# Performance work log

Measured on AMD Instinct MI355X. Metric: run time of the kernel, lower is better.

## Reference

```python
import jax, jax.numpy as jnp
import numpy as np

PAD = 0
N_WORDS, INPUT, HIDDEN, LATENT = 32000, 512, 1024, 512
B, T = 64, 512


def setup_inputs() -> dict:
    key = jax.random.key(0)
    ks = jax.random.split(key, 10)
    gin = INPUT + LATENT
    s_ih = 1.0 / np.sqrt(HIDDEN)
    inp = {
        'x': jax.random.randint(ks[0], (B, T), 0, N_WORDS, dtype=jnp.int64) if jax.config.read('jax_enable_x64') else jax.random.randint(ks[0], (B, T), 0, N_WORDS).astype(jnp.int32),
        'z': jax.random.normal(ks[1], (B, LATENT), dtype=jnp.float32),
        'emb_table': jax.random.normal(ks[2], (N_WORDS, INPUT), dtype=jnp.float32) * 0.02,
        'W_ih': jax.random.uniform(ks[3], (3 * HIDDEN, gin), minval=-s_ih, maxval=s_ih, dtype=jnp.float32),
        'b_ih': jax.random.uniform(ks[4], (3 * HIDDEN,), minval=-s_ih, maxval=s_ih, dtype=jnp.float32),
        'W_hh': jax.random.uniform(ks[5], (3 * HIDDEN, HIDDEN), minval=-s_ih, maxval=s_ih, dtype=jnp.float32),
        'b_hh': jax.random.uniform(ks[6], (3 * HIDDEN,), minval=-s_ih, maxval=s_ih, dtype=jnp.float32),
        'W_out': jax.random.uniform(ks[7], (INPUT, HIDDEN + INPUT), minval=-0.02, maxval=0.02, dtype=jnp.float32),
        'b_out': jnp.zeros((INPUT,), dtype=jnp.float32),
    }
    return inp


def _masked_gru(inp, mask, W_ih, b_ih, W_hh, b_hh):
    # inp: [B,T,Din], mask: [B,T] True at PAD positions (hidden frozen there)
    x_proj = jnp.einsum('btd,gd->btg', inp, W_ih) + b_ih  # [B,T,3H]
    xp = jnp.swapaxes(x_proj, 0, 1)                       # [T,B,3H]
    m = jnp.swapaxes(mask, 0, 1)                          # [T,B]
    h0 = jnp.zeros((inp.shape[0], HIDDEN), dtype=inp.dtype)

    def step(h, xm):
        xp_t, m_t = xm
        hp = h @ W_hh.T + b_hh
        xr, xu, xn = jnp.split(xp_t, 3, axis=-1)
        hr, hu, hn = jnp.split(hp, 3, axis=-1)
        r = jax.nn.sigmoid(xr + hr)
        u = jax.nn.sigmoid(xu + hu)
        n = jnp.tanh(xn + r * hn)
        h_new = (1.0 - u) * n + u * h
        h = jnp.where(m_t[:, None], h, h_new)
        return h, h

    _, hs = jax.lax.scan(step, h0, (xp, m))
    return jnp.swapaxes(hs, 0, 1)  # [B,T,H]


def reference(x, z, emb_table, W_ih, b_ih, W_hh, b_hh, W_out, b_out):
    mask = (x == PAD)                                  # [B,T]
    emb = emb_table[x]                                 # [B,T,INPUT]
    zt = jnp.broadcast_to(z[:, None, :], (x.shape[0], x.shape[1], z.shape[-1]))
    inp = jnp.concatenate([emb, zt], axis=-1)          # [B,T,INPUT+LATENT]
    hidden = _masked_gru(inp, mask, W_ih, b_ih, W_hh, b_hh)
    cat = jnp.concatenate([hidden, emb], axis=-1)      # [B,T,H+INPUT]
    logits = jnp.tanh(jnp.einsum('btd,od->bto', cat, W_out) + b_out)
    return logits
```

## Files before the change

### kernel.cpp

```cpp
#include <hip/hip_runtime.h>
#include <cmath>

#define PAD 0
#define INPUT 512
#define HIDDEN 1024
#define LATENT 512
#define BATCH 64
#define TLEN 512
#define G3 3072
#define GIN 1024
#define NXCD 8
#define TC 64

__global__ __launch_bounds__(256) void k_zproj(const float* __restrict__ z,
                                               const float* __restrict__ W_ih,
                                               const float* __restrict__ b_ih,
                                               float* __restrict__ zp) {
    __shared__ float zs[LATENT];
    const int b = blockIdx.y;
    const int g = blockIdx.x * 256 + threadIdx.x;
    for (int i = threadIdx.x; i < LATENT; i += 256) zs[i] = z[b * LATENT + i];
    __syncthreads();
    const float* wrow = W_ih + (size_t)g * GIN + INPUT;
    float acc = b_ih[g];
#pragma unroll 4
    for (int k = 0; k < LATENT; k += 4) {
        const float4 w = *reinterpret_cast<const float4*>(wrow + k);
        acc += zs[k] * w.x + zs[k + 1] * w.y + zs[k + 2] * w.z + zs[k + 3] * w.w;
    }
    zp[b * G3 + g] = acc;
}

__global__ void k_mask(const int* __restrict__ x, int* __restrict__ maskT) {
    const int t = blockIdx.x;
    const int b = threadIdx.x;
    maskT[t * BATCH + b] = (x[b * TLEN + t] == PAD) ? 1 : 0;
}

__global__ __launch_bounds__(256) void k_xproj(const int* __restrict__ x,
                                               const float* __restrict__ emb,
                                               const float* __restrict__ W_ih,
                                               const float* __restrict__ zp,
                                               float* __restrict__ xp,
                                               const int t_base) {
    __shared__ float smem[8448];
    __shared__ int toks[128];
    float (*As)[132] = (float(*)[132])smem;
    float (*Bs)[68]  = (float(*)[68])(smem + 4224);
    float (*Cs)[132] = (float(*)[132])smem;

    const int tid = threadIdx.x;
    const int tx = tid & 15, ty = tid >> 4;
    const int n0 = blockIdx.x * 64;
    const int m0 = blockIdx.y * 128;
    const int t0 = m0 >> 6;
    if (tid < 128) toks[tid] = x[(tid & 63) * TLEN + t_base + t0 + (tid >> 6)];
    __syncthreads();

    float acc[8][4] = {};
    for (int k0 = 0; k0 < INPUT; k0 += 32) {
        for (int idx = tid; idx < 128 * 32; idx += 256) {
            const int i = idx >> 5, kk = idx & 31;
            As[kk][i] = emb[(size_t)toks[i] * INPUT + k0 + kk];
        }
        for (int idx = tid; idx < 64 * 32; idx += 256) {
            const int i = idx >> 5, kk = idx & 31;
            Bs[kk][i] = W_ih[(size_t)(n0 + i) * GIN + k0 + kk];
        }
        __syncthreads();
#pragma unroll
        for (int kk = 0; kk < 32; ++kk) {
            const float4 a0 = *reinterpret_cast<const float4*>(&As[kk][ty * 8]);
            const float4 a1 = *reinterpret_cast<const float4*>(&As[kk][ty * 8 + 4]);
            const float4 bv = *reinterpret_cast<const float4*>(&Bs[kk][tx * 4]);
            const float av[8] = {a0.x, a0.y, a0.z, a0.w, a1.x, a1.y, a1.z, a1.w};
            const float bw[4] = {bv.x, bv.y, bv.z, bv.w};
#pragma unroll
            for (int i = 0; i < 8; ++i)
#pragma unroll
                for (int j = 0; j < 4; ++j) acc[i][j] += av[i] * bw[j];
        }
        __syncthreads();
    }
#pragma unroll
    for (int i = 0; i < 8; ++i) {
        const int b = (ty * 8 + i) & 63;
        const float4 zv = *reinterpret_cast<const float4*>(&zp[(size_t)b * G3 + n0 + tx * 4]);
        Cs[tx * 4 + 0][ty * 8 + i] = acc[i][0] + zv.x;
        Cs[tx * 4 + 1][ty * 8 + i] = acc[i][1] + zv.y;
        Cs[tx * 4 + 2][ty * 8 + i] = acc[i][2] + zv.z;
        Cs[tx * 4 + 3][ty * 8 + i] = acc[i][3] + zv.w;
    }
    __syncthreads();
#pragma unroll
    for (int it = 0; it < 32; ++it) {
        const int idx = it * 256 + tid;
        const int b = idx & 63;
        const int gl = (idx >> 6) & 63;
        const int tt = idx >> 12;
        xp[(size_t)(t0 + tt) * (G3 * BATCH) + (size_t)(n0 + gl) * BATCH + b] =
            Cs[gl][tt * 64 + b];
    }
}

__global__ __launch_bounds__(256) void k_gru_step(
    const float* __restrict__ xp_t,
    const float* __restrict__ hrep_r,
    float* __restrict__ hrep_w,
    float* __restrict__ hs_t,
    const float* __restrict__ Whh,
    const float* __restrict__ bhh,
    const int* __restrict__ maskt,
    const int t) {
    __shared__ float Ws[12 * 1024];
    __shared__ float Ab[2 * 64 * 128];

    const int tid = threadIdx.x;
    const int jl = tid >> 6;
    const int b = tid & 63;
    const int j0 = blockIdx.x * 4;
    const int j = j0 + jl;

    const float xr = xp_t[(size_t)j * BATCH + b];
    const float xu = xp_t[(size_t)(HIDDEN + j) * BATCH + b];
    const float xn = xp_t[(size_t)(2 * HIDDEN + j) * BATCH + b];
    const float* hrd = hrep_r + (size_t)(blockIdx.x & (NXCD - 1)) * (BATCH * HIDDEN);
    const float hold = (t > 0) ? hrd[b * HIDDEN + j] : 0.f;
    const int msk = maskt[b];
    const float br = bhh[j], bu = bhh[HIDDEN + j], bn = bhh[2 * HIDDEN + j];

#pragma unroll
    for (int q = 0; q < 12; ++q) {
        const int f4 = q * 256 + tid;
        const int row = f4 >> 8;
        const int col = (f4 & 255) * 4;
        const int g = (row >> 2) * HIDDEN + j0 + (row & 3);
        *reinterpret_cast<float4*>(&Ws[row * 1024 + col]) =
            *reinterpret_cast<const float4*>(&Whh[(size_t)g * HIDDEN + col]);
    }

    float ar0 = 0.f, ar1 = 0.f, au0 = 0.f, au1 = 0.f, an0 = 0.f, an1 = 0.f;

    if (t > 0) {
        float4 st[8];
        auto ldchunk = [&](int c, float4* r) {
#pragma unroll
            for (int q = 0; q < 8; ++q) {
                const int flat = q * 256 + tid;
                const int bb = flat >> 5;
                const int kc = (flat & 31) * 4;
                const int ks = kc ^ ((bb & 7) << 2);
                r[q] = *reinterpret_cast<const float4*>(
                    &hrd[(size_t)bb * HIDDEN + c * 128 + ks]);
            }
        };
        auto stchunk = [&](int buf, const float4* r) {
            float* A = Ab + buf * (64 * 128);
#pragma unroll
            for (int q = 0; q < 8; ++q) {
                const int flat = q * 256 + tid;
                *reinterpret_cast<float4*>(&A[flat * 4]) = r[q];
            }
        };

        ldchunk(0, st);
        stchunk(0, st);
        __syncthreads();

        const int swz = (b & 7) << 2;
        const float* wrb = Ws + (0 * 4 + jl) * 1024;
        const float* wub = Ws + (4 + jl) * 1024;
        const float* wnb = Ws + (8 + jl) * 1024;

        for (int c = 0; c < 8; ++c) {
            if (c < 7) ldchunk(c + 1, st);
            const float* A = Ab + (c & 1) * (64 * 128) + b * 128;
            const float* wr = wrb + c * 128;
            const float* wu = wub + c * 128;
            const float* wn = wnb + c * 128;
#pragma unroll
            for (int kk = 0; kk < 128; kk += 8) {
                const float4 h0 = *reinterpret_cast<const float4*>(&A[kk ^ swz]);
                const float4 h1 = *reinterpret_cast<const float4*>(&A[(kk + 4) ^ swz]);
                const float4 r0 = *reinterpret_cast<const float4*>(&wr[kk]);
                const float4 r1 = *reinterpret_cast<const float4*>(&wr[kk + 4]);
                const float4 u0 = *reinterpret_cast<const float4*>(&wu[kk]);
                const float4 u1 = *reinterpret_cast<const float4*>(&wu[kk + 4]);
                const float4 n0v = *reinterpret_cast<const float4*>(&wn[kk]);
                const float4 n1v = *reinterpret_cast<const float4*>(&wn[kk + 4]);
                ar0 += h0.x * r0.x + h0.y * r0.y + h0.z * r0.z + h0.w * r0.w;
                ar1 += h1.x * r1.x + h1.y * r1.y + h1.z * r1.z + h1.w * r1.w;
                au0 += h0.x * u0.x + h0.y * u0.y + h0.z * u0.z + h0.w * u0.w;
                au1 += h1.x * u1.x + h1.y * u1.y + h1.z * u1.z + h1.w * u1.w;
                an0 += h0.x * n0v.x + h0.y * n0v.y + h0.z * n0v.z + h0.w * n0v.w;
                an1 += h1.x * n1v.x + h1.y * n1v.y + h1.z * n1v.z + h1.w * n1v.w;
            }
            if (c < 7) {
                stchunk((c + 1) & 1, st);
                __syncthreads();
            }
        }
    }

    const float hr = ar0 + ar1 + br;
    const float hu = au0 + au1 + bu;
    const float hn = an0 + an1 + bn;
    const float r = 1.f / (1.f + expf(-(xr + hr)));
    const float u = 1.f / (1.f + expf(-(xu + hu)));
    const float n = tanhf(xn + r * hn);
    float hnew = (1.f - u) * n + u * hold;
    if (msk) hnew = hold;

#pragma unroll
    for (int rep = 0; rep < NXCD; ++rep)
        hrep_w[(size_t)rep * (BATCH * HIDDEN) + (size_t)b * HIDDEN + j] = hnew;
    hs_t[(size_t)b * HIDDEN + j] = hnew;
}

__global__ __launch_bounds__(256) void k_out(const float* __restrict__ hs,
                                             const int* __restrict__ x,
                                             const float* __restrict__ emb,
                                             const float* __restrict__ W_out,
                                             const float* __restrict__ b_out,
                                             float* __restrict__ out,
                                             const int t_base) {
    __shared__ float As[32][132];
    __shared__ float Bs[32][68];
    __shared__ int toks[128];
    const int tid = threadIdx.x;
    const int tx = tid & 15, ty = tid >> 4;
    const int n0 = blockIdx.x * 64;
    const int m0 = blockIdx.y * 128;
    const int t0 = m0 >> 6;
    if (tid < 128) toks[tid] = x[(tid & 63) * TLEN + t_base + t0 + (tid >> 6)];
    __syncthreads();

    float acc[8][4] = {};
    for (int k0 = 0; k0 < HIDDEN + INPUT; k0 += 32) {
        if (k0 < HIDDEN) {
            for (int idx = tid; idx < 128 * 32; idx += 256) {
                const int i = idx >> 5, kk = idx & 31;
                As[kk][i] = hs[(size_t)(m0 + i) * HIDDEN + k0 + kk];
            }
        } else {
            for (int idx = tid; idx < 128 * 32; idx += 256) {
                const int i = idx >> 5, kk = idx & 31;
                As[kk][i] = emb[(size_t)toks[i] * INPUT + (k0 - HIDDEN) + kk];
            }
        }
        for (int idx = tid; idx < 64 * 32; idx += 256) {
            const int i = idx >> 5, kk = idx & 31;
            Bs[kk][i] = W_out[(size_t)(n0 + i) * (HIDDEN + INPUT) + k0 + kk];
        }
        __syncthreads();
#pragma unroll
        for (int kk = 0; kk < 32; ++kk) {
            const float4 a0 = *reinterpret_cast<const float4*>(&As[kk][ty * 8]);
            const float4 a1 = *reinterpret_cast<const float4*>(&As[kk][ty * 8 + 4]);
            const float4 bv = *reinterpret_cast<const float4*>(&Bs[kk][tx * 4]);
            const float av[8] = {a0.x, a0.y, a0.z, a0.w, a1.x, a1.y, a1.z, a1.w};
            const float bw[4] = {bv.x, bv.y, bv.z, bv.w};
#pragma unroll
            for (int i = 0; i < 8; ++i)
#pragma unroll
                for (int j = 0; j < 4; ++j) acc[i][j] += av[i] * bw[j];
        }
        __syncthreads();
    }
    const float4 bo = *reinterpret_cast<const float4*>(&b_out[n0 + tx * 4]);
    const float bof[4] = {bo.x, bo.y, bo.z, bo.w};
#pragma unroll
    for (int i = 0; i < 8; ++i) {
        const int ml = m0 + ty * 8 + i;
        const int b = ml & 63;
        const int t = t_base + (ml >> 6);
        float4 o;
        o.x = tanhf(acc[i][0] + bof[0]);
        o.y = tanhf(acc[i][1] + bof[1]);
        o.z = tanhf(acc[i][2] + bof[2]);
        o.w = tanhf(acc[i][3] + bof[3]);
        *reinterpret_cast<float4*>(
            &out[(size_t)b * (TLEN * INPUT) + (size_t)t * INPUT + n0 + tx * 4]) = o;
    }
}

extern "C" void kernel_launch(void* const* d_in, const int* in_sizes, int n_in,
                              void* d_out, int out_size, void* d_ws, size_t ws_size,
                              hipStream_t stream) {
    const int* x = (const int*)d_in[0];
    const float* z = (const float*)d_in[1];
    const float* emb = (const float*)d_in[2];
    const float* W_ih = (const float*)d_in[3];
    const float* b_ih = (const float*)d_in[4];
    const float* W_hh = (const float*)d_in[5];
    const float* b_hh = (const float*)d_in[6];
    const float* W_out = (const float*)d_in[7];
    const float* b_out = (const float*)d_in[8];
    float* out = (float*)d_out;

    float* xp = (float*)d_ws;
    float* hsbuf = xp + (size_t)TC * G3 * BATCH;
    float* hrepA = hsbuf + (size_t)TC * BATCH * HIDDEN;
    float* hrepB = hrepA + (size_t)NXCD * BATCH * HIDDEN;
    float* zp = hrepB + (size_t)NXCD * BATCH * HIDDEN;
    int* maskT = (int*)(zp + (size_t)BATCH * G3);

    k_zproj<<<dim3(G3 / 256, BATCH), 256, 0, stream>>>(z, W_ih, b_ih, zp);
    k_mask<<<TLEN, BATCH, 0, stream>>>(x, maskT);

    for (int c = 0; c < TLEN / TC; ++c) {
        const int tb = c * TC;
        k_xproj<<<dim3(G3 / 64, TC * BATCH / 128), 256, 0, stream>>>(
            x, emb, W_ih, zp, xp, tb);
        for (int tl = 0; tl < TC; ++tl) {
            const int t = tb + tl;
            const float* hr = (t & 1) ? hrepA : hrepB;
            float* hw = (t & 1) ? hrepB : hrepA;
            k_gru_step<<<256, 256, 0, stream>>>(
                xp + (size_t)tl * G3 * BATCH, hr, hw,
                hsbuf + (size_t)tl * BATCH * HIDDEN,
                W_hh, b_hh, maskT + t * BATCH, t);
        }
        k_out<<<dim3(INPUT / 64, TC * BATCH / 128), 256, 0, stream>>>(
            hsbuf, x, emb, W_out, b_out, out, tb);
    }
}
```

Before: 38.80 ms.

## Run GRU time chunk as persistent cooperative kernel with grid sync

Replaces the 64 per-timestep GRU kernel launches per chunk with one cooperative kernel that stages W_hh slices into shared memory once and loops over timesteps, using grid.sync between steps. It also drops the per-XCD hidden-state replication in favour of a single ping-pong buffer pair, and shrinks the K chunk for the h tile to 32 with a single shared buffer. This removes launch overhead and repeated W_hh reloads, at the cost of grid-wide barrier latency and more __syncthreads per step. A per-step-launch fallback is kept if the cooperative launch fails.

```diff
diff --git a/kernel.cpp b/kernel.cpp
--- a/kernel.cpp
+++ b/kernel.cpp
@@ -1,5 +1,8 @@
 #include <hip/hip_runtime.h>
+#include <hip/hip_cooperative_groups.h>
 #include <cmath>
+
+namespace cg = cooperative_groups;
 
 #define PAD 0
 #define INPUT 512
@@ -9,8 +12,8 @@
 #define TLEN 512
 #define G3 3072
 #define GIN 1024
-#define NXCD 8
 #define TC 64
+#define KC 32
 
 __global__ __launch_bounds__(256) void k_zproj(const float* __restrict__ z,
                                                const float* __restrict__ W_ih,
@@ -103,32 +106,8 @@
     }
 }
 
-__global__ __launch_bounds__(256) void k_gru_step(
-    const float* __restrict__ xp_t,
-    const float* __restrict__ hrep_r,
-    float* __restrict__ hrep_w,
-    float* __restrict__ hs_t,
-    const float* __restrict__ Whh,
-    const float* __restrict__ bhh,
-    const int* __restrict__ maskt,
-    const int t) {
-    __shared__ float Ws[12 * 1024];
-    __shared__ float Ab[2 * 64 * 128];
-
-    const int tid = threadIdx.x;
-    const int jl = tid >> 6;
-    const int b = tid & 63;
-    const int j0 = blockIdx.x * 4;
-    const int j = j0 + jl;
-
-    const float xr = xp_t[(size_t)j * BATCH + b];
-    const float xu = xp_t[(size_t)(HIDDEN + j) * BATCH + b];
-    const float xn = xp_t[(size_t)(2 * HIDDEN + j) * BATCH + b];
-    const float* hrd = hrep_r + (size_t)(blockIdx.x & (NXCD - 1)) * (BATCH * HIDDEN);
-    const float hold = (t > 0) ? hrd[b * HIDDEN + j] : 0.f;
-    const int msk = maskt[b];
-    const float br = bhh[j], bu = bhh[HIDDEN + j], bn = bhh[2 * HIDDEN + j];
-
+__device__ __forceinline__ void stage_Ws(const float* __restrict__ Whh,
+                                         float* Ws, int tid, int j0) {
 #pragma unroll
     for (int q = 0; q < 12; ++q) {
         const int f4 = q * 256 + tid;
@@ -138,48 +117,61 @@
         *reinterpret_cast<float4*>(&Ws[row * 1024 + col]) =
             *reinterpret_cast<const float4*>(&Whh[(size_t)g * HIDDEN + col]);
     }
+}
+
+__device__ __forceinline__ void gru_step(
+    const float* __restrict__ xpt,
+    const float* __restrict__ hin,
+    float* __restrict__ hout,
+    float* __restrict__ hsl,
+    const float* Ws, float* Ab,
+    const int* __restrict__ maskt,
+    float br, float bu, float bn,
+    int t, int tid, int jl, int b, int j) {
+
+    const float xr = xpt[(size_t)j * BATCH + b];
+    const float xu = xpt[(size_t)(HIDDEN + j) * BATCH + b];
+    const float xn = xpt[(size_t)(2 * HIDDEN + j) * BATCH + b];
+    const int msk = maskt[b];
+    const float hold = (t > 0) ? hin[(size_t)b * HIDDEN + j] : 0.f;
 
     float ar0 = 0.f, ar1 = 0.f, au0 = 0.f, au1 = 0.f, an0 = 0.f, an1 = 0.f;
 
     if (t > 0) {
-        float4 st[8];
-        auto ldchunk = [&](int c, float4* r) {
-#pragma unroll
-            for (int q = 0; q < 8; ++q) {
+        float4 st[2];
+        auto ldchunk = [&](int c) {
+#pragma unroll
+            for (int q = 0; q < 2; ++q) {
                 const int flat = q * 256 + tid;
-                const int bb = flat >> 5;
-                const int kc = (flat & 31) * 4;
+                const int bb = flat >> 3;
+                const int kc = (flat & 7) * 4;
                 const int ks = kc ^ ((bb & 7) << 2);
-                r[q] = *reinterpret_cast<const float4*>(
-                    &hrd[(size_t)bb * HIDDEN + c * 128 + ks]);
+                st[q] = *reinterpret_cast<const float4*>(
+                    &hin[(size_t)bb * HIDDEN + c * KC + ks]);
             }
         };
-        auto stchunk = [&](int buf, const float4* r) {
-            float* A = Ab + buf * (64 * 128);
-#pragma unroll
-            for (int q = 0; q < 8; ++q) {
-                const int flat = q * 256 + tid;
-                *reinterpret_cast<float4*>(&A[flat * 4]) = r[q];
-            }
-        };
-
-        ldchunk(0, st);
-        stchunk(0, st);
-        __syncthreads();
-
+
+        ldchunk(0);
         const int swz = (b & 7) << 2;
-        const float* wrb = Ws + (0 * 4 + jl) * 1024;
+        const float* wrb = Ws + jl * 1024;
         const float* wub = Ws + (4 + jl) * 1024;
         const float* wnb = Ws + (8 + jl) * 1024;
 
-        for (int c = 0; c < 8; ++c) {
-            if (c < 7) ldchunk(c + 1, st);
-            const float* A = Ab + (c & 1) * (64 * 128) + b * 128;
-            const float* wr = wrb + c * 128;
-            const float* wu = wub + c * 128;
-            const float* wn = wnb + c * 128;
-#pragma unroll
-            for (int kk = 0; kk < 128; kk += 8) {
+        for (int c = 0; c < HIDDEN / KC; ++c) {
+            __syncthreads();
+#pragma unroll
+            for (int q = 0; q < 2; ++q) {
+                const int flat = q * 256 + tid;
+                *reinterpret_cast<float4*>(&Ab[flat * 4]) = st[q];
+            }
+            if (c < HIDDEN / KC - 1) ldchunk(c + 1);
+            __syncthreads();
+            const float* A = Ab + b * KC;
+            const float* wr = wrb + c * KC;
+            const float* wu = wub + c * KC;
+            const float* wn = wnb + c * KC;
+#pragma unroll
+            for (int kk = 0; kk < KC; kk += 8) {
                 const float4 h0 = *reinterpret_cast<const float4*>(&A[kk ^ swz]);
                 const float4 h1 = *reinterpret_cast<const float4*>(&A[(kk + 4) ^ swz]);
                 const float4 r0 = *reinterpret_cast<const float4*>(&wr[kk]);
@@ -195,10 +187,6 @@
                 an0 += h0.x * n0v.x + h0.y * n0v.y + h0.z * n0v.z + h0.w * n0v.w;
                 an1 += h1.x * n1v.x + h1.y * n1v.y + h1.z * n1v.z + h1.w * n1v.w;
             }
-            if (c < 7) {
-                stchunk((c + 1) & 1, st);
-                __syncthreads();
-            }
         }
     }
 
@@ -211,10 +199,62 @@
     float hnew = (1.f - u) * n + u * hold;
     if (msk) hnew = hold;
 
-#pragma unroll
-    for (int rep = 0; rep < NXCD; ++rep)
-        hrep_w[(size_t)rep * (BATCH * HIDDEN) + (size_t)b * HIDDEN + j] = hnew;
-    hs_t[(size_t)b * HIDDEN + j] = hnew;
+    hout[(size_t)b * HIDDEN + j] = hnew;
+    hsl[(size_t)b * HIDDEN + j] = hnew;
+}
+
+__global__ __launch_bounds__(256) void k_gru_chunk(
+    const float* __restrict__ xp,
+    float* __restrict__ buf0,
+    float* __restrict__ buf1,
+    float* __restrict__ hsbuf,
+    const float* __restrict__ Whh,
+    const float* __restrict__ bhh,
+    const int* __restrict__ maskT,
+    const int t_base) {
+    __shared__ float Ws[12 * 1024];
+    __shared__ float Ab[64 * KC];
+    cg::grid_group grid = cg::this_grid();
+
+    const int tid = threadIdx.x;
+    const int jl = tid >> 6;
+    const int b = tid & 63;
+    const int j0 = blockIdx.x * 4;
+    const int j = j0 + jl;
+
+    stage_Ws(Whh, Ws, tid, j0);
+    const float br = bhh[j], bu = bhh[HIDDEN + j], bn = bhh[2 * HIDDEN + j];
+
+    for (int tl = 0; tl < TC; ++tl) {
+        const int t = t_base + tl;
+        const float* hin = (t & 1) ? buf0 : buf1;
+        float* hout = (t & 1) ? buf1 : buf0;
+        gru_step(xp + (size_t)tl * (G3 * BATCH), hin, hout,
+                 hsbuf + (size_t)tl * (BATCH * HIDDEN),
+                 Ws, Ab, maskT + t * BATCH, br, bu, bn, t, tid, jl, b, j);
+        grid.sync();
+    }
+}
+
+__global__ __launch_bounds__(256) void k_gru_step_kern(
+    const float* __restrict__ xpt,
+    const float* __restrict__ hin,
+    float* __restrict__ hout,
+    float* __restrict__ hsl,
+    const float* __restrict__ Whh,
+    const float* __restrict__ bhh,
+    const int* __restrict__ maskt,
+    const int t) {
+    __shared__ float Ws[12 * 1024];
+    __shared__ float Ab[64 * KC];
+    const int tid = threadIdx.x;
+    const int jl = tid >> 6;
+    const int b = tid & 63;
+    const int j0 = blockIdx.x * 4;
+    const int j = j0 + jl;
+    stage_Ws(Whh, Ws, tid, j0);
+    const float br = bhh[j], bu = bhh[HIDDEN + j], bn = bhh[2 * HIDDEN + j];
+    gru_step(xpt, hin, hout, hsl, Ws, Ab, maskt, br, bu, bn, t, tid, jl, b, j);
 }
 
 __global__ __launch_bounds__(256) void k_out(const float* __restrict__ hs,
@@ -300,10 +340,15 @@
 
     float* xp = (float*)d_ws;
     float* hsbuf = xp + (size_t)TC * G3 * BATCH;
-    float* hrepA = hsbuf + (size_t)TC * BATCH * HIDDEN;
-    float* hrepB = hrepA + (size_t)NXCD * BATCH * HIDDEN;
-    float* zp = hrepB + (size_t)NXCD * BATCH * HIDDEN;
+    float* buf0 = hsbuf + (size_t)TC * BATCH * HIDDEN;
+    float* buf1 = buf0 + (size_t)BATCH * HIDDEN;
+    float* zp = buf1 + (size_t)BATCH * HIDDEN;
     int* maskT = (int*)(zp + (size_t)BATCH * G3);
+
+    int nb = 0;
+    hipError_t qe = hipOccupancyMaxActiveBlocksPerMultiprocessor(
+        &nb, k_gru_chunk, 256, 0);
+    const bool coop_ok = (qe == hipSuccess && nb >= 1);
 
     k_zproj<<<dim3(G3 / 256, BATCH), 256, 0, stream>>>(z, W_ih, b_ih, zp);
     k_mask<<<TLEN, BATCH, 0, stream>>>(x, maskT);
@@ -312,15 +357,28 @@
         const int tb = c * TC;
         k_xproj<<<dim3(G3 / 64, TC * BATCH / 128), 256, 0, stream>>>(
             x, emb, W_ih, zp, xp, tb);
-        for (int tl = 0; tl < TC; ++tl) {
-            const int t = tb + tl;
-            const float* hr = (t & 1) ? hrepA : hrepB;
-            float* hw = (t & 1) ? hrepB : hrepA;
-            k_gru_step<<<256, 256, 0, stream>>>(
-                xp + (size_t)tl * G3 * BATCH, hr, hw,
-                hsbuf + (size_t)tl * BATCH * HIDDEN,
-                W_hh, b_hh, maskT + t * BATCH, t);
-        }
+
+        bool done = false;
+        if (coop_ok) {
+            int tb_arg = tb;
+            void* args[] = {(void*)&xp, (void*)&buf0, (void*)&buf1, (void*)&hsbuf,
+                            (void*)&W_hh, (void*)&b_hh, (void*)&maskT, (void*)&tb_arg};
+            hipError_t le = hipLaunchCooperativeKernel(
+                (const void*)k_gru_chunk, dim3(256), dim3(256), args, 0, stream);
+            done = (le == hipSuccess);
+        }
+        if (!done) {
+            for (int tl = 0; tl < TC; ++tl) {
+                const int t = tb + tl;
+                const float* hin = (t & 1) ? buf0 : buf1;
+                float* hout = (t & 1) ? buf1 : buf0;
+                k_gru_step_kern<<<256, 256, 0, stream>>>(
+                    xp + (size_t)tl * G3 * BATCH, hin, hout,
+                    hsbuf + (size_t)tl * BATCH * HIDDEN,
+                    W_hh, b_hh, maskT + t * BATCH, t);
+            }
+        }
+
         k_out<<<dim3(INPUT / 64, TC * BATCH / 128), 256, 0, stream>>>(
             hsbuf, x, emb, W_out, b_out, out, tb);
     }
```

Result: faster. 36.39 ms (-6.2%).
